# Kernel tuning notes

Hardware: AMD Instinct MI355X
Metric: run time of the kernel (lower is better)

Reference implementation:

```python
import jax, jax.numpy as jnp
import numpy as np

N_NODES = 200_000
N_BONDS = 200_000
N_EDGES = 2 * N_BONDS
D_V, D_E, D_H, DEPTH = 133, 14, 200, 3


def setup_inputs() -> dict:
    key = jax.random.key(0)
    ks = jax.random.split(key, 10)
    V = jax.random.normal(ks[0], (N_NODES, D_V), dtype=jnp.float32)
    E_feat = jax.random.normal(ks[1], (N_EDGES, D_E), dtype=jnp.float32)
    # paired directed edges: edge 2b = (u,v), edge 2b+1 = (v,u)
    u = jax.random.randint(ks[2], (N_BONDS,), 0, N_NODES)
    v = jax.random.randint(ks[3], (N_BONDS,), 0, N_NODES)
    src = jnp.stack([u, v], axis=1).reshape(-1)
    dst = jnp.stack([v, u], axis=1).reshape(-1)
    edge_index = jnp.stack([src, dst], axis=0).astype(jnp.int64)
    rev_edge_index = (jnp.arange(N_EDGES) ^ 1).astype(jnp.int64)
    s = 0.05
    W_i = jax.random.normal(ks[4], (D_V + D_E, D_H), dtype=jnp.float32) * s
    b_i = jax.random.normal(ks[5], (D_H,), dtype=jnp.float32) * s
    W_h = jax.random.normal(ks[6], (D_H, D_H), dtype=jnp.float32) * s
    b_h = jax.random.normal(ks[7], (D_H,), dtype=jnp.float32) * s
    W_o = jax.random.normal(ks[8], (D_V + D_H, D_H), dtype=jnp.float32) * s
    b_o = jax.random.normal(ks[9], (D_H,), dtype=jnp.float32) * s
    return {"V": V, "E_feat": E_feat, "edge_index": edge_index,
            "rev_edge_index": rev_edge_index, "W_i": W_i, "b_i": b_i,
            "W_h": W_h, "b_h": b_h, "W_o": W_o, "b_o": b_o}


def reference(V, E_feat, edge_index, rev_edge_index, W_i, b_i, W_h, b_h, W_o, b_o):
    src = edge_index[0]
    dst = edge_index[1]
    n_edges = E_feat.shape[0]
    # h^(0) = relu(W_i([x_v || e_vw]))
    H0 = jax.nn.relu(jnp.concatenate([V[src], E_feat], axis=1) @ W_i + b_i)
    H = H0
    not_self_rev = (rev_edge_index != jnp.arange(n_edges))[:, None]  # [E,1]
    for _ in range(1, DEPTH):
        node_messages = jax.ops.segment_sum(H, dst, num_segments=N_NODES)  # [N,d_h]
        M = node_messages[src] - jnp.where(not_self_rev, H[rev_edge_index], 0.0)
        H = jax.nn.relu(H0 + M @ W_h + b_h)
    M_v = jax.ops.segment_sum(H, src, num_segments=N_NODES)  # [N,d_h]
    H_v = jax.nn.relu(jnp.concatenate([V, M_v], axis=1) @ W_o + b_o)
    return H_v
```

## Files before the change

### kernel.cpp

```cpp
#include <hip/hip_runtime.h>
#include <hip/hip_bf16.h>
#include <stdint.h>

typedef __hip_bfloat16 bf16;
typedef __attribute__((ext_vector_type(8))) short short8;
typedef __attribute__((ext_vector_type(4))) float f32x4;

#define NN 200000
#define NNPAD 200064
#define NE 400000
#define DV 133
#define DE 14
#define DH 200
#define MT 128
#define NT 13
#define NCH 782

#define CI 5
#define CH 7
#define CO 11
#define KO 352
#define LDV 160

#define MFMA(a, b, c) __builtin_amdgcn_mfma_f32_16x16x32_bf16((a), (b), (c), 0, 0, 0)

__device__ __forceinline__ float us2f(unsigned short u) {
  return __uint_as_float(((unsigned)u) << 16);
}
__device__ __forceinline__ unsigned short f2us(float f) {
  bf16 h = __float2bfloat16(f);
  return *reinterpret_cast<unsigned short*>(&h);
}

__global__ __launch_bounds__(256) void prepwpack_kernel(
    const float* __restrict__ W, int Ksrc, int nchunks, int mode,
    unsigned short* __restrict__ out)
{
  int f = blockIdx.x * 256 + threadIdx.x;
  int total = nchunks * 13 * 64;
  if (f >= total) return;
  int c = f / 832, rem = f - c * 832;
  int t = rem >> 6, l = rem & 63;
  int q = l >> 4, ln = l & 15;
  int col = t * 16 + ln;
  short8 w;
#pragma unroll
  for (int j = 0; j < 8; ++j) {
    int k = c * 32 + q * 8 + j;
    float v = 0.f;
    if (col < DH) {
      if (mode == 0) {
        if (k < Ksrc) v = W[(size_t)k * DH + col];
      } else {
        if (k < 333) {
          int sr = (k < 200) ? (133 + k) : (k - 200);
          v = W[(size_t)sr * DH + col];
        }
      }
    }
    w[j] = (short)f2us(v);
  }
  *(short8*)&out[(size_t)f * 8] = w;
}

__global__ __launch_bounds__(256) void packv_kernel(
    const float* __restrict__ V, unsigned short* __restrict__ Vb)
{
  int idx = blockIdx.x * 256 + threadIdx.x;
  if (idx >= NN * (LDV / 8)) return;
  int n = idx / (LDV / 8), g = idx - n * (LDV / 8);
  int k0 = g * 8;
  short8 w;
#pragma unroll
  for (int j = 0; j < 8; ++j) {
    int k = k0 + j;
    float v = (k < DV) ? V[(size_t)n * DV + k] : 0.f;
    w[j] = (short)f2us(v);
  }
  *(short8*)&Vb[(size_t)n * LDV + k0] = w;
}

__global__ __launch_bounds__(256) void packet_kernel(
    const float* __restrict__ V, const float* __restrict__ Ef,
    const int* __restrict__ src, unsigned short* __restrict__ Et)
{
  int idx = blockIdx.x * 256 + threadIdx.x;
  if (idx >= NE * 4) return;
  int e = idx >> 2, part = idx & 3;
  short8 w;
#pragma unroll
  for (int j = 0; j < 8; ++j) w[j] = 0;
  if (part == 0) {
    int s = src[e];
#pragma unroll
    for (int j = 0; j < 5; ++j) w[j] = (short)f2us(V[(size_t)s * DV + 128 + j]);
#pragma unroll
    for (int j = 5; j < 8; ++j) w[j] = (short)f2us(Ef[(size_t)e * DE + (j - 5)]);
  } else if (part == 1) {
#pragma unroll
    for (int j = 0; j < 8; ++j) w[j] = (short)f2us(Ef[(size_t)e * DE + 3 + j]);
  } else if (part == 2) {
#pragma unroll
    for (int j = 0; j < 3; ++j) w[j] = (short)f2us(Ef[(size_t)e * DE + 11 + j]);
  }
  *(short8*)&Et[(size_t)e * 32 + part * 8] = w;
}

__global__ __launch_bounds__(256) void packav_kernel(
    const float* __restrict__ V, unsigned short* __restrict__ Abuf)
{
  int idx = blockIdx.x * 256 + threadIdx.x;
  if (idx >= NNPAD * (KO / 8)) return;
  int n = idx / (KO / 8), g = idx - n * (KO / 8);
  int k0 = g * 8;
  if (n < NN && k0 < 200) return;
  short8 w;
#pragma unroll
  for (int j = 0; j < 8; ++j) {
    int k = k0 + j;
    float v = (n < NN && k >= 200 && k < 333) ? V[(size_t)n * DV + (k - 200)] : 0.f;
    w[j] = (short)f2us(v);
  }
  *(short8*)&Abuf[(size_t)n * KO + k0] = w;
}

__global__ __launch_bounds__(256) void hist_kernel(
    const int* __restrict__ dst, int* __restrict__ counts)
{
  int e = blockIdx.x * 256 + threadIdx.x;
  if (e < NE) atomicAdd(&counts[dst[e]], 1);
}

__global__ __launch_bounds__(256) void chunksum_kernel(
    const int* __restrict__ counts, int* __restrict__ chunkSum)
{
  int b = blockIdx.x, tid = threadIdx.x;
  int i = b * 256 + tid;
  int v = (i < NN) ? counts[i] : 0;
#pragma unroll
  for (int d = 32; d; d >>= 1) v += __shfl_down(v, d, 64);
  __shared__ int ws[4];
  if ((tid & 63) == 0) ws[tid >> 6] = v;
  __syncthreads();
  if (tid == 0) chunkSum[b] = ws[0] + ws[1] + ws[2] + ws[3];
}

__global__ __launch_bounds__(1024) void scanchunks_kernel(
    const int* __restrict__ chunkSum, int* __restrict__ chunkOff)
{
  __shared__ int s[1024];
  int tid = threadIdx.x;
  int v = (tid < NCH) ? chunkSum[tid] : 0;
  s[tid] = v;
  __syncthreads();
  for (int d = 1; d < 1024; d <<= 1) {
    int t = (tid >= d) ? s[tid - d] : 0;
    __syncthreads();
    s[tid] += t;
    __syncthreads();
  }
  if (tid < NCH) chunkOff[tid] = s[tid] - v;
}

__global__ __launch_bounds__(256) void scanlocal_kernel(
    const int* __restrict__ counts, const int* __restrict__ chunkOff,
    int* __restrict__ offsets, int* __restrict__ cursor)
{
  __shared__ int s[256];
  int b = blockIdx.x, tid = threadIdx.x;
  int i = b * 256 + tid;
  int v = (i < NN) ? counts[i] : 0;
  s[tid] = v;
  __syncthreads();
  for (int d = 1; d < 256; d <<= 1) {
    int t = (tid >= d) ? s[tid - d] : 0;
    __syncthreads();
    s[tid] += t;
    __syncthreads();
  }
  if (i < NN) {
    int off = chunkOff[b] + s[tid] - v;
    offsets[i] = off;
    cursor[i] = off;
  }
  if (i == 0) offsets[NN] = NE;
}

__global__ __launch_bounds__(256) void scatter_kernel(
    const int* __restrict__ dst, int* __restrict__ cursor, int* __restrict__ perm)
{
  int e = blockIdx.x * 256 + threadIdx.x;
  if (e < NE) {
    int p = atomicAdd(&cursor[dst[e]], 1);
    perm[p] = e;
  }
}

__global__ __launch_bounds__(256) void h0_kernel(
    const unsigned short* __restrict__ Vb,
    const unsigned short* __restrict__ Et,
    const int* __restrict__ src,
    const unsigned short* __restrict__ Bp,
    const float* __restrict__ bi,
    bf16* __restrict__ H0)
{
  __shared__ float Sb[DH];
  const int tid = threadIdx.x;
  const int e0 = blockIdx.x * MT;
  if (tid < DH) Sb[tid] = bi[tid];
  const int wv = tid >> 6, ln = tid & 15, q = (tid & 63) >> 4;
  const int lane = tid & 63;
  __syncthreads();
  f32x4 acc[NT][2];
#pragma unroll
  for (int t = 0; t < NT; ++t)
#pragma unroll
    for (int m = 0; m < 2; ++m) acc[t][m] = (f32x4){0.f, 0.f, 0.f, 0.f};
  const int r0 = wv * 32 + ln;
  const int s0 = src[e0 + r0], s1 = src[e0 + r0 + 16];
  const unsigned short* v0p = Vb + (size_t)s0 * LDV;
  const unsigned short* v1p = Vb + (size_t)s1 * LDV;
  const unsigned short* bp = Bp + (size_t)lane * 8;
  short8 bfr[NT];
#pragma unroll
  for (int c = 0; c < 4; ++c) {
    short8 a0 = *(const short8*)(v0p + c * 32 + q * 8);
    short8 a1 = *(const short8*)(v1p + c * 32 + q * 8);
#pragma unroll
    for (int t = 0; t < NT; ++t)
      bfr[t] = *(const short8*)(bp + (size_t)(c * NT + t) * 512);
#pragma unroll
    for (int t = 0; t < NT; ++t) {
      acc[t][0] = MFMA(a0, bfr[t], acc[t][0]);
      acc[t][1] = MFMA(a1, bfr[t], acc[t][1]);
    }
  }
  {
    short8 a0 = *(const short8*)(Et + (size_t)(e0 + r0) * 32 + q * 8);
    short8 a1 = *(const short8*)(Et + (size_t)(e0 + r0 + 16) * 32 + q * 8);
#pragma unroll
    for (int t = 0; t < NT; ++t)
      bfr[t] = *(const short8*)(bp + (size_t)(4 * NT + t) * 512);
#pragma unroll
    for (int t = 0; t < NT; ++t) {
      acc[t][0] = MFMA(a0, bfr[t], acc[t][0]);
      acc[t][1] = MFMA(a1, bfr[t], acc[t][1]);
    }
  }
#pragma unroll
  for (int t = 0; t < NT; ++t) {
    int c = t * 16 + ln;
    if (c < DH) {
#pragma unroll
      for (int m = 0; m < 2; ++m)
#pragma unroll
        for (int i = 0; i < 4; ++i) {
          int e = e0 + wv * 32 + m * 16 + q * 4 + i;
          float h = acc[t][m][i] + Sb[c];
          H0[(size_t)e * DH + c] = __float2bfloat16(h > 0.f ? h : 0.f);
        }
    }
  }
}

__global__ __launch_bounds__(256) void gemmq_kernel(
    const bf16* __restrict__ H,
    const unsigned short* __restrict__ Bp,
    bf16* __restrict__ Q)
{
  const int tid = threadIdx.x;
  const int e0 = blockIdx.x * MT;
  const int wv = tid >> 6, ln = tid & 15, q = (tid & 63) >> 4;
  const int lane = tid & 63;
  f32x4 acc[NT][2];
#pragma unroll
  for (int t = 0; t < NT; ++t)
#pragma unroll
    for (int m = 0; m < 2; ++m) acc[t][m] = (f32x4){0.f, 0.f, 0.f, 0.f};
  const unsigned short* Hs = (const unsigned short*)H;
  const unsigned short* a0p = Hs + (size_t)(e0 + wv * 32 + ln) * DH;
  const unsigned short* a1p = a0p + (size_t)16 * DH;
  const unsigned short* bp = Bp + (size_t)lane * 8;
  short8 bfr[NT];
#pragma unroll
  for (int c = 0; c < CH; ++c) {
    short8 a0 = *(const short8*)(a0p + c * 32 + q * 8);
    short8 a1 = *(const short8*)(a1p + c * 32 + q * 8);
#pragma unroll
    for (int t = 0; t < NT; ++t)
      bfr[t] = *(const short8*)(bp + (size_t)(c * NT + t) * 512);
#pragma unroll
    for (int t = 0; t < NT; ++t) {
      acc[t][0] = MFMA(a0, bfr[t], acc[t][0]);
      acc[t][1] = MFMA(a1, bfr[t], acc[t][1]);
    }
  }
#pragma unroll
  for (int t = 0; t < NT; ++t) {
    int c = t * 16 + ln;
    if (c < DH) {
#pragma unroll
      for (int m = 0; m < 2; ++m)
#pragma unroll
        for (int i = 0; i < 4; ++i) {
          int e = e0 + wv * 32 + m * 16 + q * 4 + i;
          Q[(size_t)e * DH + c] = __float2bfloat16(acc[t][m][i]);
        }
    }
  }
}

__global__ __launch_bounds__(256) void fusedmp_kernel(
    const bf16* __restrict__ Q, const bf16* H0,
    const int* __restrict__ offsets, const int* __restrict__ perm,
    const float* __restrict__ bh, bf16* Hout)
{
  int t = blockIdx.x * 256 + threadIdx.x;
  if (t >= NN * 25) return;
  int n = t / 25, g = t - n * 25;
  int st = offsets[n], en = offsets[n + 1];
  if (st == en) return;
  const unsigned short* Qs = (const unsigned short*)Q;
  const unsigned short* H0s = (const unsigned short*)H0;
  unsigned short* Os = (unsigned short*)Hout;
  float a[8];
  const float4* bp = (const float4*)(bh + g * 8);
  float4 b0 = bp[0], b1 = bp[1];
  a[0] = b0.x; a[1] = b0.y; a[2] = b0.z; a[3] = b0.w;
  a[4] = b1.x; a[5] = b1.y; a[6] = b1.z; a[7] = b1.w;
  for (int j = st; j < en; ++j) {
    int e = perm[j];
    short8 u = *(const short8*)(Qs + (size_t)e * DH + g * 8);
#pragma unroll
    for (int k = 0; k < 8; ++k) a[k] += us2f((unsigned short)u[k]);
  }
  for (int j = st; j < en; ++j) {
    int e = perm[j];
    int eo = e ^ 1;
    short8 uq = *(const short8*)(Qs + (size_t)e * DH + g * 8);
    short8 uh = *(const short8*)(H0s + (size_t)eo * DH + g * 8);
    short8 w;
#pragma unroll
    for (int k = 0; k < 8; ++k) {
      float h = a[k] - us2f((unsigned short)uq[k]) + us2f((unsigned short)uh[k]);
      w[k] = (short)f2us(h > 0.f ? h : 0.f);
    }
    *(short8*)(Os + (size_t)eo * DH + g * 8) = w;
  }
}

__global__ __launch_bounds__(256) void gather_kernel(
    const bf16* __restrict__ H, const int* __restrict__ offsets,
    const int* __restrict__ perm, int xm, unsigned short* __restrict__ Abuf)
{
  int t = blockIdx.x * 256 + threadIdx.x;
  if (t >= NN * 25) return;
  int n = t / 25, g = t - n * 25;
  int st = offsets[n], en = offsets[n + 1];
  float a[8];
#pragma unroll
  for (int k = 0; k < 8; ++k) a[k] = 0.f;
  const unsigned short* Hs = (const unsigned short*)H;
  for (int j = st; j < en; ++j) {
    int e = perm[j] ^ xm;
    short8 u = *(const short8*)(Hs + (size_t)e * DH + g * 8);
#pragma unroll
    for (int k = 0; k < 8; ++k) a[k] += us2f((unsigned short)u[k]);
  }
  short8 w;
#pragma unroll
  for (int k = 0; k < 8; ++k) w[k] = (short)f2us(a[k]);
  *(short8*)&Abuf[(size_t)n * KO + g * 8] = w;
}

__global__ __launch_bounds__(256) void out_kernel(
    const unsigned short* __restrict__ Abuf,
    const unsigned short* __restrict__ Bp,
    const float* __restrict__ bo,
    float* __restrict__ out)
{
  __shared__ float Sb[DH];
  const int tid = threadIdx.x;
  const int n0 = blockIdx.x * MT;
  if (tid < DH) Sb[tid] = bo[tid];
  const int wv = tid >> 6, ln = tid & 15, q = (tid & 63) >> 4;
  const int lane = tid & 63;
  __syncthreads();
  f32x4 acc[NT][2];
#pragma unroll
  for (int t = 0; t < NT; ++t)
#pragma unroll
    for (int m = 0; m < 2; ++m) acc[t][m] = (f32x4){0.f, 0.f, 0.f, 0.f};
  const unsigned short* a0p = Abuf + (size_t)(n0 + wv * 32 + ln) * KO;
  const unsigned short* a1p = a0p + (size_t)16 * KO;
  const unsigned short* bp = Bp + (size_t)lane * 8;
  short8 bfr[NT];
#pragma unroll
  for (int c = 0; c < CO; ++c) {
    short8 a0 = *(const short8*)(a0p + c * 32 + q * 8);
    short8 a1 = *(const short8*)(a1p + c * 32 + q * 8);
#pragma unroll
    for (int t = 0; t < NT; ++t)
      bfr[t] = *(const short8*)(bp + (size_t)(c * NT + t) * 512);
#pragma unroll
    for (int t = 0; t < NT; ++t) {
      acc[t][0] = MFMA(a0, bfr[t], acc[t][0]);
      acc[t][1] = MFMA(a1, bfr[t], acc[t][1]);
    }
  }
#pragma unroll
  for (int t = 0; t < NT; ++t) {
    int c = t * 16 + ln;
    if (c < DH) {
#pragma unroll
      for (int m = 0; m < 2; ++m)
#pragma unroll
        for (int i = 0; i < 4; ++i) {
          int n = n0 + wv * 32 + m * 16 + q * 4 + i;
          if (n < NN) {
            float h = acc[t][m][i] + Sb[c];
            out[(size_t)n * DH + c] = h > 0.f ? h : 0.f;
          }
        }
    }
  }
}

extern "C" void kernel_launch(void* const* d_in, const int* in_sizes, int n_in,
                              void* d_out, int out_size, void* d_ws, size_t ws_size,
                              hipStream_t stream)
{
  const float* V  = (const float*)d_in[0];
  const float* Ef = (const float*)d_in[1];
  const int* eidx = (const int*)d_in[2];
  const int* rev  = (const int*)d_in[3];   (void)rev;
  const float* Wi = (const float*)d_in[4];
  const float* bi = (const float*)d_in[5];
  const float* Wh = (const float*)d_in[6];
  const float* bh = (const float*)d_in[7];
  const float* Wo = (const float*)d_in[8];
  const float* bo = (const float*)d_in[9];
  const int* src = eidx;
  const int* dst = eidx + NE;

  bf16* H0 = (bf16*)d_ws;
  bf16* Hb = H0 + (size_t)NE * DH;
  bf16* Q  = Hb + (size_t)NE * DH;
  unsigned short* Vb16 = (unsigned short*)Hb;
  unsigned short* Et   = (unsigned short*)Q;
  unsigned short* Abuf = (unsigned short*)Q;
  int* counts   = (int*)(Q + (size_t)NE * DH);
  int* chunkSum = counts + NN;
  int* chunkOff = chunkSum + 1024;
  int* offsets  = chunkOff + 1024;
  int* cursor   = offsets + NN + 1;
  int* perm     = cursor + NN;
  unsigned short* Bpi = (unsigned short*)(((uintptr_t)(perm + NE) + 15) & ~(uintptr_t)15);
  unsigned short* Bph = Bpi + (size_t)CI * 832 * 8;
  unsigned short* Bpo = Bph + (size_t)CH * 832 * 8;

  const int gGE = NE / MT;
  const int gON = (NN + MT - 1) / MT;
  const int gE  = (NE + 255) / 256;
  const int gN  = (NN + 255) / 256;
  const int gG  = (NN * 25 + 255) / 256;

  hipMemsetAsync(counts, 0, (size_t)NN * sizeof(int), stream);
  hist_kernel<<<gE, 256, 0, stream>>>(dst, counts);
  chunksum_kernel<<<NCH, 256, 0, stream>>>(counts, chunkSum);
  scanchunks_kernel<<<1, 1024, 0, stream>>>(chunkSum, chunkOff);
  scanlocal_kernel<<<gN, 256, 0, stream>>>(counts, chunkOff, offsets, cursor);
  scatter_kernel<<<gE, 256, 0, stream>>>(dst, cursor, perm);

  prepwpack_kernel<<<(CI * 832 + 255) / 256, 256, 0, stream>>>(Wi, DV + DE, CI, 0, Bpi);
  prepwpack_kernel<<<(CH * 832 + 255) / 256, 256, 0, stream>>>(Wh, DH, CH, 0, Bph);
  prepwpack_kernel<<<(CO * 832 + 255) / 256, 256, 0, stream>>>(Wo, 0, CO, 1, Bpo);

  packv_kernel<<<(NN * (LDV / 8) + 255) / 256, 256, 0, stream>>>(V, Vb16);
  packet_kernel<<<(NE * 4 + 255) / 256, 256, 0, stream>>>(V, Ef, src, Et);

  h0_kernel<<<gGE, 256, 0, stream>>>(Vb16, Et, src, Bpi, bi, H0);

  gemmq_kernel<<<gGE, 256, 0, stream>>>(H0, Bph, Q);
  fusedmp_kernel<<<gG, 256, 0, stream>>>(Q, H0, offsets, perm, bh, Hb);

  gemmq_kernel<<<gGE, 256, 0, stream>>>(Hb, Bph, Q);
  fusedmp_kernel<<<gG, 256, 0, stream>>>(Q, H0, offsets, perm, bh, H0);

  packav_kernel<<<(NNPAD * (KO / 8) + 255) / 256, 256, 0, stream>>>(V, Abuf);

  gather_kernel<<<gG, 256, 0, stream>>>(H0, offsets, perm, 1, Abuf);
  out_kernel<<<gON, 256, 0, stream>>>(Abuf, Bpo, bo, (float*)d_out);
}
```

Baseline: 1.283 ms.

## Aggregate node sums before GEMM and fuse message update into GEMM epilogue

Each message-passing layer changes order. Instead of computing Q = H·W_h for every edge and then gathering and scattering Q per node, it first gathers H into per-node bf16 sums S. A single GEMM kernel then computes (S[src] − H[rev])·W_h, using two MFMAs per tile with a sign-flipped reverse-edge operand, and adds bias, H0 and ReLU in the epilogue. This removes the separate Q write and the double Q gather pass, in exchange for twice the MFMA work, gathered reads of S rows inside the GEMM, and extra bf16 rounding of the node sums before subtraction.

```diff
diff --git a/kernel.cpp b/kernel.cpp
--- a/kernel.cpp
+++ b/kernel.cpp
@@ -5,6 +5,7 @@
 typedef __hip_bfloat16 bf16;
 typedef __attribute__((ext_vector_type(8))) short short8;
 typedef __attribute__((ext_vector_type(4))) float f32x4;
+typedef __attribute__((ext_vector_type(4))) int int4v;
 
 #define NN 200000
 #define NNPAD 200064
@@ -21,6 +22,7 @@
 #define CO 11
 #define KO 352
 #define LDV 160
+#define LDS_ 224
 
 #define MFMA(a, b, c) __builtin_amdgcn_mfma_f32_16x16x32_bf16((a), (b), (c), 0, 0, 0)
 
@@ -30,6 +32,11 @@
 __device__ __forceinline__ unsigned short f2us(float f) {
   bf16 h = __float2bfloat16(f);
   return *reinterpret_cast<unsigned short*>(&h);
+}
+__device__ __forceinline__ short8 neg8(short8 x) {
+  int4v v = *(int4v*)&x;
+  v ^= (int)0x80008000;
+  return *(short8*)&v;
 }
 
 __global__ __launch_bounds__(256) void prepwpack_kernel(
@@ -263,38 +270,85 @@
   }
 }
 
-__global__ __launch_bounds__(256) void gemmq_kernel(
+__global__ __launch_bounds__(256) void gsum_kernel(
+    const bf16* __restrict__ H, const int* __restrict__ offsets,
+    const int* __restrict__ perm, unsigned short* __restrict__ S)
+{
+  int t = blockIdx.x * 256 + threadIdx.x;
+  if (t >= NN * 28) return;
+  int n = t / 28, g = t - n * 28;
+  short8 w;
+  if (g >= 25) {
+#pragma unroll
+    for (int k = 0; k < 8; ++k) w[k] = 0;
+    *(short8*)&S[(size_t)n * LDS_ + g * 8] = w;
+    return;
+  }
+  int st = offsets[n], en = offsets[n + 1];
+  float a[8];
+#pragma unroll
+  for (int k = 0; k < 8; ++k) a[k] = 0.f;
+  const unsigned short* Hs = (const unsigned short*)H;
+  for (int j = st; j < en; ++j) {
+    int e = perm[j];
+    short8 u = *(const short8*)(Hs + (size_t)e * DH + g * 8);
+#pragma unroll
+    for (int k = 0; k < 8; ++k) a[k] += us2f((unsigned short)u[k]);
+  }
+#pragma unroll
+  for (int k = 0; k < 8; ++k) w[k] = (short)f2us(a[k]);
+  *(short8*)&S[(size_t)n * LDS_ + g * 8] = w;
+}
+
+__global__ __launch_bounds__(256) void fmp_kernel(
     const bf16* __restrict__ H,
+    const bf16* H0,
+    const unsigned short* __restrict__ S,
+    const int* __restrict__ src,
     const unsigned short* __restrict__ Bp,
-    bf16* __restrict__ Q)
-{
+    const float* __restrict__ bh,
+    bf16* Hout)
+{
+  __shared__ float Sb[DH];
   const int tid = threadIdx.x;
   const int e0 = blockIdx.x * MT;
+  if (tid < DH) Sb[tid] = bh[tid];
   const int wv = tid >> 6, ln = tid & 15, q = (tid & 63) >> 4;
   const int lane = tid & 63;
+  __syncthreads();
   f32x4 acc[NT][2];
 #pragma unroll
   for (int t = 0; t < NT; ++t)
 #pragma unroll
     for (int m = 0; m < 2; ++m) acc[t][m] = (f32x4){0.f, 0.f, 0.f, 0.f};
+  const int r0 = e0 + wv * 32 + ln, r1 = r0 + 16;
+  const int s0 = src[r0], s1 = src[r1];
+  const unsigned short* sp0 = S + (size_t)s0 * LDS_;
+  const unsigned short* sp1 = S + (size_t)s1 * LDS_;
   const unsigned short* Hs = (const unsigned short*)H;
-  const unsigned short* a0p = Hs + (size_t)(e0 + wv * 32 + ln) * DH;
-  const unsigned short* a1p = a0p + (size_t)16 * DH;
+  const unsigned short* hp0 = Hs + (size_t)(r0 ^ 1) * DH;
+  const unsigned short* hp1 = Hs + (size_t)(r1 ^ 1) * DH;
   const unsigned short* bp = Bp + (size_t)lane * 8;
   short8 bfr[NT];
 #pragma unroll
   for (int c = 0; c < CH; ++c) {
-    short8 a0 = *(const short8*)(a0p + c * 32 + q * 8);
-    short8 a1 = *(const short8*)(a1p + c * 32 + q * 8);
+    short8 sa0 = *(const short8*)(sp0 + c * 32 + q * 8);
+    short8 sa1 = *(const short8*)(sp1 + c * 32 + q * 8);
+    short8 na0 = neg8(*(const short8*)(hp0 + c * 32 + q * 8));
+    short8 na1 = neg8(*(const short8*)(hp1 + c * 32 + q * 8));
 #pragma unroll
     for (int t = 0; t < NT; ++t)
       bfr[t] = *(const short8*)(bp + (size_t)(c * NT + t) * 512);
 #pragma unroll
     for (int t = 0; t < NT; ++t) {
-      acc[t][0] = MFMA(a0, bfr[t], acc[t][0]);
-      acc[t][1] = MFMA(a1, bfr[t], acc[t][1]);
-    }
-  }
+      acc[t][0] = MFMA(sa0, bfr[t], acc[t][0]);
+      acc[t][0] = MFMA(na0, bfr[t], acc[t][0]);
+      acc[t][1] = MFMA(sa1, bfr[t], acc[t][1]);
+      acc[t][1] = MFMA(na1, bfr[t], acc[t][1]);
+    }
+  }
+  const unsigned short* H0s = (const unsigned short*)H0;
+  unsigned short* Os = (unsigned short*)Hout;
 #pragma unroll
   for (int t = 0; t < NT; ++t) {
     int c = t * 16 + ln;
@@ -304,48 +358,10 @@
 #pragma unroll
         for (int i = 0; i < 4; ++i) {
           int e = e0 + wv * 32 + m * 16 + q * 4 + i;
-          Q[(size_t)e * DH + c] = __float2bfloat16(acc[t][m][i]);
+          float h = acc[t][m][i] + Sb[c] + us2f(H0s[(size_t)e * DH + c]);
+          Os[(size_t)e * DH + c] = f2us(h > 0.f ? h : 0.f);
         }
     }
-  }
-}
-
-__global__ __launch_bounds__(256) void fusedmp_kernel(
-    const bf16* __restrict__ Q, const bf16* H0,
-    const int* __restrict__ offsets, const int* __restrict__ perm,
-    const float* __restrict__ bh, bf16* Hout)
-{
-  int t = blockIdx.x * 256 + threadIdx.x;
-  if (t >= NN * 25) return;
-  int n = t / 25, g = t - n * 25;
-  int st = offsets[n], en = offsets[n + 1];
-  if (st == en) return;
-  const unsigned short* Qs = (const unsigned short*)Q;
-  const unsigned short* H0s = (const unsigned short*)H0;
-  unsigned short* Os = (unsigned short*)Hout;
-  float a[8];
-  const float4* bp = (const float4*)(bh + g * 8);
-  float4 b0 = bp[0], b1 = bp[1];
-  a[0] = b0.x; a[1] = b0.y; a[2] = b0.z; a[3] = b0.w;
-  a[4] = b1.x; a[5] = b1.y; a[6] = b1.z; a[7] = b1.w;
-  for (int j = st; j < en; ++j) {
-    int e = perm[j];
-    short8 u = *(const short8*)(Qs + (size_t)e * DH + g * 8);
-#pragma unroll
-    for (int k = 0; k < 8; ++k) a[k] += us2f((unsigned short)u[k]);
-  }
-  for (int j = st; j < en; ++j) {
-    int e = perm[j];
-    int eo = e ^ 1;
-    short8 uq = *(const short8*)(Qs + (size_t)e * DH + g * 8);
-    short8 uh = *(const short8*)(H0s + (size_t)eo * DH + g * 8);
-    short8 w;
-#pragma unroll
-    for (int k = 0; k < 8; ++k) {
-      float h = a[k] - us2f((unsigned short)uq[k]) + us2f((unsigned short)uh[k]);
-      w[k] = (short)f2us(h > 0.f ? h : 0.f);
-    }
-    *(short8*)(Os + (size_t)eo * DH + g * 8) = w;
   }
 }
 
@@ -445,11 +461,12 @@
 
   bf16* H0 = (bf16*)d_ws;
   bf16* Hb = H0 + (size_t)NE * DH;
-  bf16* Q  = Hb + (size_t)NE * DH;
+  bf16* R3 = Hb + (size_t)NE * DH;
   unsigned short* Vb16 = (unsigned short*)Hb;
-  unsigned short* Et   = (unsigned short*)Q;
-  unsigned short* Abuf = (unsigned short*)Q;
-  int* counts   = (int*)(Q + (size_t)NE * DH);
+  unsigned short* Et   = (unsigned short*)R3;
+  unsigned short* Sbuf = (unsigned short*)R3;
+  unsigned short* Abuf = (unsigned short*)R3;
+  int* counts   = (int*)(R3 + (size_t)NE * DH);
   int* chunkSum = counts + NN;
   int* chunkOff = chunkSum + 1024;
   int* offsets  = chunkOff + 1024;
@@ -464,6 +481,7 @@
   const int gE  = (NE + 255) / 256;
   const int gN  = (NN + 255) / 256;
   const int gG  = (NN * 25 + 255) / 256;
+  const int gS  = (NN * 28 + 255) / 256;
 
   hipMemsetAsync(counts, 0, (size_t)NN * sizeof(int), stream);
   hist_kernel<<<gE, 256, 0, stream>>>(dst, counts);
@@ -481,11 +499,11 @@
 
   h0_kernel<<<gGE, 256, 0, stream>>>(Vb16, Et, src, Bpi, bi, H0);
 
-  gemmq_kernel<<<gGE, 256, 0, stream>>>(H0, Bph, Q);
-  fusedmp_kernel<<<gG, 256, 0, stream>>>(Q, H0, offsets, perm, bh, Hb);
-
-  gemmq_kernel<<<gGE, 256, 0, stream>>>(Hb, Bph, Q);
-  fusedmp_kernel<<<gG, 256, 0, stream>>>(Q, H0, offsets, perm, bh, H0);
+  gsum_kernel<<<gS, 256, 0, stream>>>(H0, offsets, perm, Sbuf);
+  fmp_kernel<<<gGE, 256, 0, stream>>>(H0, H0, Sbuf, src, Bph, bh, Hb);
+
+  gsum_kernel<<<gS, 256, 0, stream>>>(Hb, offsets, perm, Sbuf);
+  fmp_kernel<<<gGE, 256, 0, stream>>>(Hb, H0, Sbuf, src, Bph, bh, H0);
 
   packav_kernel<<<(NNPAD * (KO / 8) + 255) / 256, 256, 0, stream>>>(V, Abuf);
 
```

Measured after the change: 1.890 ms. +47.3%, slower.

## Store edge features in dst-sorted order to make message-passing reads sequential

Applied to the files above, without the earlier changes.

Edges are renumbered into CSR (dst-sorted) order, and inverse and reverse-position arrays are built so that H0, Q and H are stored in that order. The per-node reductions in fusedmp and the final gather then read Q and H contiguously instead of going through perm indirection. The last pass writes its output sequentially into a separate buffer (Hrev) so the final gather is a streaming read. The cost is two extra small index kernels plus three extra int arrays, and the reverse-edge H0 read and the first-pass write remain scattered.

```diff
diff --git a/kernel.cpp b/kernel.cpp
--- a/kernel.cpp
+++ b/kernel.cpp
@@ -82,16 +82,18 @@
 
 __global__ __launch_bounds__(256) void packet_kernel(
     const float* __restrict__ V, const float* __restrict__ Ef,
-    const int* __restrict__ src, unsigned short* __restrict__ Et)
+    const int* __restrict__ perm, const int* __restrict__ psrc,
+    unsigned short* __restrict__ Et)
 {
   int idx = blockIdx.x * 256 + threadIdx.x;
   if (idx >= NE * 4) return;
-  int e = idx >> 2, part = idx & 3;
+  int p = idx >> 2, part = idx & 3;
+  int e = perm[p];
   short8 w;
 #pragma unroll
   for (int j = 0; j < 8; ++j) w[j] = 0;
   if (part == 0) {
-    int s = src[e];
+    int s = psrc[p];
 #pragma unroll
     for (int j = 0; j < 5; ++j) w[j] = (short)f2us(V[(size_t)s * DV + 128 + j]);
 #pragma unroll
@@ -103,7 +105,7 @@
 #pragma unroll
     for (int j = 0; j < 3; ++j) w[j] = (short)f2us(Ef[(size_t)e * DE + 11 + j]);
   }
-  *(short8*)&Et[(size_t)e * 32 + part * 8] = w;
+  *(short8*)&Et[(size_t)p * 32 + part * 8] = w;
 }
 
 __global__ __launch_bounds__(256) void packav_kernel(
@@ -196,10 +198,29 @@
   }
 }
 
+__global__ __launch_bounds__(256) void invperm_kernel(
+    const int* __restrict__ perm, int* __restrict__ ipos)
+{
+  int p = blockIdx.x * 256 + threadIdx.x;
+  if (p < NE) ipos[perm[p]] = p;
+}
+
+__global__ __launch_bounds__(256) void rpos_kernel(
+    const int* __restrict__ perm, const int* __restrict__ ipos,
+    const int* __restrict__ src, int* __restrict__ rpos, int* __restrict__ psrc)
+{
+  int p = blockIdx.x * 256 + threadIdx.x;
+  if (p < NE) {
+    int e = perm[p];
+    rpos[p] = ipos[e ^ 1];
+    psrc[p] = src[e];
+  }
+}
+
 __global__ __launch_bounds__(256) void h0_kernel(
     const unsigned short* __restrict__ Vb,
     const unsigned short* __restrict__ Et,
-    const int* __restrict__ src,
+    const int* __restrict__ psrc,
     const unsigned short* __restrict__ Bp,
     const float* __restrict__ bi,
     bf16* __restrict__ H0)
@@ -217,7 +238,7 @@
 #pragma unroll
     for (int m = 0; m < 2; ++m) acc[t][m] = (f32x4){0.f, 0.f, 0.f, 0.f};
   const int r0 = wv * 32 + ln;
-  const int s0 = src[e0 + r0], s1 = src[e0 + r0 + 16];
+  const int s0 = psrc[e0 + r0], s1 = psrc[e0 + r0 + 16];
   const unsigned short* v0p = Vb + (size_t)s0 * LDV;
   const unsigned short* v1p = Vb + (size_t)s1 * LDV;
   const unsigned short* bp = Bp + (size_t)lane * 8;
@@ -311,9 +332,9 @@
 }
 
 __global__ __launch_bounds__(256) void fusedmp_kernel(
-    const bf16* __restrict__ Q, const bf16* H0,
-    const int* __restrict__ offsets, const int* __restrict__ perm,
-    const float* __restrict__ bh, bf16* Hout)
+    const bf16* __restrict__ Q, const bf16* __restrict__ H0,
+    const int* __restrict__ offsets, const int* __restrict__ rpos,
+    const float* __restrict__ bh, int seqout, bf16* __restrict__ Hout)
 {
   int t = blockIdx.x * 256 + threadIdx.x;
   if (t >= NN * 25) return;
@@ -328,30 +349,28 @@
   float4 b0 = bp[0], b1 = bp[1];
   a[0] = b0.x; a[1] = b0.y; a[2] = b0.z; a[3] = b0.w;
   a[4] = b1.x; a[5] = b1.y; a[6] = b1.z; a[7] = b1.w;
-  for (int j = st; j < en; ++j) {
-    int e = perm[j];
-    short8 u = *(const short8*)(Qs + (size_t)e * DH + g * 8);
+  for (int p = st; p < en; ++p) {
+    short8 u = *(const short8*)(Qs + (size_t)p * DH + g * 8);
 #pragma unroll
     for (int k = 0; k < 8; ++k) a[k] += us2f((unsigned short)u[k]);
   }
-  for (int j = st; j < en; ++j) {
-    int e = perm[j];
-    int eo = e ^ 1;
-    short8 uq = *(const short8*)(Qs + (size_t)e * DH + g * 8);
-    short8 uh = *(const short8*)(H0s + (size_t)eo * DH + g * 8);
+  for (int p = st; p < en; ++p) {
+    int rp = rpos[p];
+    short8 uq = *(const short8*)(Qs + (size_t)p * DH + g * 8);
+    short8 uh = *(const short8*)(H0s + (size_t)rp * DH + g * 8);
     short8 w;
 #pragma unroll
     for (int k = 0; k < 8; ++k) {
       float h = a[k] - us2f((unsigned short)uq[k]) + us2f((unsigned short)uh[k]);
       w[k] = (short)f2us(h > 0.f ? h : 0.f);
     }
-    *(short8*)(Os + (size_t)eo * DH + g * 8) = w;
-  }
-}
-
-__global__ __launch_bounds__(256) void gather_kernel(
-    const bf16* __restrict__ H, const int* __restrict__ offsets,
-    const int* __restrict__ perm, int xm, unsigned short* __restrict__ Abuf)
+    *(short8*)(Os + (size_t)(seqout ? p : rp) * DH + g * 8) = w;
+  }
+}
+
+__global__ __launch_bounds__(256) void gatherseq_kernel(
+    const bf16* __restrict__ Hrev, const int* __restrict__ offsets,
+    unsigned short* __restrict__ Abuf)
 {
   int t = blockIdx.x * 256 + threadIdx.x;
   if (t >= NN * 25) return;
@@ -360,10 +379,9 @@
   float a[8];
 #pragma unroll
   for (int k = 0; k < 8; ++k) a[k] = 0.f;
-  const unsigned short* Hs = (const unsigned short*)H;
-  for (int j = st; j < en; ++j) {
-    int e = perm[j] ^ xm;
-    short8 u = *(const short8*)(Hs + (size_t)e * DH + g * 8);
+  const unsigned short* Hs = (const unsigned short*)Hrev;
+  for (int p = st; p < en; ++p) {
+    short8 u = *(const short8*)(Hs + (size_t)p * DH + g * 8);
 #pragma unroll
     for (int k = 0; k < 8; ++k) a[k] += us2f((unsigned short)u[k]);
   }
@@ -447,6 +465,7 @@
   bf16* Hb = H0 + (size_t)NE * DH;
   bf16* Q  = Hb + (size_t)NE * DH;
   unsigned short* Vb16 = (unsigned short*)Hb;
+  bf16* Hrev = Hb;
   unsigned short* Et   = (unsigned short*)Q;
   unsigned short* Abuf = (unsigned short*)Q;
   int* counts   = (int*)(Q + (size_t)NE * DH);
@@ -455,7 +474,10 @@
   int* offsets  = chunkOff + 1024;
   int* cursor   = offsets + NN + 1;
   int* perm     = cursor + NN;
-  unsigned short* Bpi = (unsigned short*)(((uintptr_t)(perm + NE) + 15) & ~(uintptr_t)15);
+  int* ipos     = perm + NE;
+  int* rpos     = ipos + NE;
+  int* psrc     = rpos + NE;
+  unsigned short* Bpi = (unsigned short*)(((uintptr_t)(psrc + NE) + 15) & ~(uintptr_t)15);
   unsigned short* Bph = Bpi + (size_t)CI * 832 * 8;
   unsigned short* Bpo = Bph + (size_t)CH * 832 * 8;
 
@@ -471,24 +493,26 @@
   scanchunks_kernel<<<1, 1024, 0, stream>>>(chunkSum, chunkOff);
   scanlocal_kernel<<<gN, 256, 0, stream>>>(counts, chunkOff, offsets, cursor);
   scatter_kernel<<<gE, 256, 0, stream>>>(dst, cursor, perm);
+  invperm_kernel<<<gE, 256, 0, stream>>>(perm, ipos);
+  rpos_kernel<<<gE, 256, 0, stream>>>(perm, ipos, src, rpos, psrc);
 
   prepwpack_kernel<<<(CI * 832 + 255) / 256, 256, 0, stream>>>(Wi, DV + DE, CI, 0, Bpi);
   prepwpack_kernel<<<(CH * 832 + 255) / 256, 256, 0, stream>>>(Wh, DH, CH, 0, Bph);
   prepwpack_kernel<<<(CO * 832 + 255) / 256, 256, 0, stream>>>(Wo, 0, CO, 1, Bpo);
 
   packv_kernel<<<(NN * (LDV / 8) + 255) / 256, 256, 0, stream>>>(V, Vb16);
-  packet_kernel<<<(NE * 4 + 255) / 256, 256, 0, stream>>>(V, Ef, src, Et);
-
-  h0_kernel<<<gGE, 256, 0, stream>>>(Vb16, Et, src, Bpi, bi, H0);
+  packet_kernel<<<(NE * 4 + 255) / 256, 256, 0, stream>>>(V, Ef, perm, psrc, Et);
+
+  h0_kernel<<<gGE, 256, 0, stream>>>(Vb16, Et, psrc, Bpi, bi, H0);
 
   gemmq_kernel<<<gGE, 256, 0, stream>>>(H0, Bph, Q);
-  fusedmp_kernel<<<gG, 256, 0, stream>>>(Q, H0, offsets, perm, bh, Hb);
+  fusedmp_kernel<<<gG, 256, 0, stream>>>(Q, H0, offsets, rpos, bh, 0, Hb);
 
   gemmq_kernel<<<gGE, 256, 0, stream>>>(Hb, Bph, Q);
-  fusedmp_kernel<<<gG, 256, 0, stream>>>(Q, H0, offsets, perm, bh, H0);
+  fusedmp_kernel<<<gG, 256, 0, stream>>>(Q, H0, offsets, rpos, bh, 1, Hrev);
 
   packav_kernel<<<(NNPAD * (KO / 8) + 255) / 256, 256, 0, stream>>>(V, Abuf);
 
-  gather_kernel<<<gG, 256, 0, stream>>>(H0, offsets, perm, 1, Abuf);
+  gatherseq_kernel<<<gG, 256, 0, stream>>>(Hrev, offsets, Abuf);
   out_kernel<<<gON, 256, 0, stream>>>(Abuf, Bpo, bo, (float*)d_out);
 }
```

Measured after the change: 1.237 ms. 3.5% less time.
